# Optimization experiments

Hardware: AMD Instinct MI355X
Metric: run time of the kernel (lower is better)

Reference implementation:

```python
import jax, jax.numpy as jnp
import numpy as np

N = 5000  # num_nodes = feature dim = num classes
E = 160000


def _gcn_conv(x, src, dst, W, b, n):
    # PyG GCNConv: h = D^{-1/2} (A + I) D^{-1/2} (x W) + b
    h = x @ W  # [n, out]
    loops = jnp.arange(n, dtype=src.dtype)
    s = jnp.concatenate([src, loops])
    d = jnp.concatenate([dst, loops])
    deg = jax.ops.segment_sum(jnp.ones_like(s, dtype=h.dtype), d, num_segments=n)
    inv_sqrt = jnp.where(deg > 0, jax.lax.rsqrt(deg), 0.0)
    coef = inv_sqrt[s] * inv_sqrt[d]  # [E+n]
    msgs = h[s] * coef[:, None]       # gather-scale
    out = jax.ops.segment_sum(msgs, d, num_segments=n)  # scatter-add
    return out + b


def setup_inputs() -> dict:
    key = jax.random.key(0)
    k1, k2, k3, k4, k5 = jax.random.split(key, 5)
    x = jax.random.normal(k1, (N, N), dtype=jnp.float32)
    src = jax.random.randint(k2, (E,), 0, N, dtype=jnp.int32)
    dst = jax.random.randint(k3, (E,), 0, N, dtype=jnp.int32)
    W1 = jax.random.normal(k4, (N, 16), dtype=jnp.float32) * (1.0 / np.sqrt(N))
    b1 = jnp.zeros((16,), dtype=jnp.float32)
    W2 = jax.random.normal(k5, (16, N), dtype=jnp.float32) * (1.0 / np.sqrt(16))
    b2 = jnp.zeros((N,), dtype=jnp.float32)
    return {"x": x, "src": src, "dst": dst, "W1": W1, "b1": b1, "W2": W2, "b2": b2}


def reference(x, src, dst, W1, b1, W2, b2):
    h = _gcn_conv(x, src, dst, W1, b1, N)
    h = jax.nn.relu(h)
    h = _gcn_conv(h, src, dst, W2, b2, N)
    return jax.nn.log_softmax(h, axis=1)
```

## Files before the change

kernel.cpp:

```cpp
#include <hip/hip_runtime.h>
#include <math.h>

#define NN 5000
#define NE 160000
#define NF 16
#define CK 256


__global__ void k_deg(const int* __restrict__ dst, float* __restrict__ deg) {
  int t = blockIdx.x * 256 + threadIdx.x;
  if (t < NE) atomicAdd(&deg[dst[t]], 1.0f);
}

__global__ void k_inv(float* __restrict__ deg) {
  int v = blockIdx.x * 256 + threadIdx.x;
  if (v < NN) deg[v] = rsqrtf(deg[v] + 1.0f);
}

__global__ __launch_bounds__(256) void k_gemm1(const float* __restrict__ x,
                                               const float* __restrict__ w1,
                                               float* __restrict__ h1) {
  __shared__ float xs[16 * CK];
  __shared__ float ws[CK * NF];
  const int tid = threadIdx.x;
  const int lane = tid & 63;
  const int wv = tid >> 6;
  const int kk = lane >> 2;
  const int jq = lane & 3;
  const int rowbase = blockIdx.x * 16;
  const int kbeg = blockIdx.y * 1252;
  const int kend = (kbeg + 1252 < NN) ? kbeg + 1252 : NN;

  float acc[16];
#pragma unroll
  for (int i = 0; i < 16; ++i) acc[i] = 0.f;

  const int srow = tid >> 4;
  const int sf4 = tid & 15;
  const int grow = rowbase + srow;
  const float* __restrict__ xrow = x + (size_t)grow * NN;

  for (int kc = kbeg; kc < kend; kc += CK) {
    __syncthreads();
#pragma unroll
    for (int p = 0; p < 4; ++p) {
      const int s4 = sf4 + 16 * p;
      const int col = kc + s4 * 4;
      float4 v = make_float4(0.f, 0.f, 0.f, 0.f);
      if (grow < NN && col + 4 <= kend) v = *(const float4*)(xrow + col);
      *(float4*)(&xs[srow * CK + s4 * 4]) = v;
    }
    {
      const int k = kc + tid;
      if (k < kend) {
        const float4* __restrict__ wr = (const float4*)(w1 + (size_t)k * NF);
#pragma unroll
        for (int q = 0; q < 4; ++q) *(float4*)(&ws[tid * NF + q * 4]) = wr[q];
      } else {
#pragma unroll
        for (int q = 0; q < 4; ++q)
          *(float4*)(&ws[tid * NF + q * 4]) = make_float4(0.f, 0.f, 0.f, 0.f);
      }
    }
    __syncthreads();
    const float* __restrict__ xb = &xs[(wv * 4) * CK + kk];
    const float* __restrict__ wb = &ws[kk * NF + jq * 4];
#pragma unroll
    for (int c = 0; c < 16; ++c) {
      const float4 w4 = *(const float4*)(wb + c * (16 * NF));
      const float x0 = xb[0 * CK + c * 16];
      const float x1 = xb[1 * CK + c * 16];
      const float x2 = xb[2 * CK + c * 16];
      const float x3 = xb[3 * CK + c * 16];
      acc[0] = fmaf(x0, w4.x, acc[0]);  acc[1] = fmaf(x0, w4.y, acc[1]);
      acc[2] = fmaf(x0, w4.z, acc[2]);  acc[3] = fmaf(x0, w4.w, acc[3]);
      acc[4] = fmaf(x1, w4.x, acc[4]);  acc[5] = fmaf(x1, w4.y, acc[5]);
      acc[6] = fmaf(x1, w4.z, acc[6]);  acc[7] = fmaf(x1, w4.w, acc[7]);
      acc[8] = fmaf(x2, w4.x, acc[8]);  acc[9] = fmaf(x2, w4.y, acc[9]);
      acc[10] = fmaf(x2, w4.z, acc[10]); acc[11] = fmaf(x2, w4.w, acc[11]);
      acc[12] = fmaf(x3, w4.x, acc[12]); acc[13] = fmaf(x3, w4.y, acc[13]);
      acc[14] = fmaf(x3, w4.z, acc[14]); acc[15] = fmaf(x3, w4.w, acc[15]);
    }
  }

  int len = 16;
#pragma unroll
  for (int m = 32; m >= 4; m >>= 1) {
    len >>= 1;
    const bool hi = (lane & m) != 0;
#pragma unroll
    for (int i = 0; i < len; ++i) {
      float keep = hi ? acc[i + len] : acc[i];
      float give = hi ? acc[i] : acc[i + len];
      acc[i] = keep + __shfl_xor(give, m);
    }
  }
  const int r = kk >> 2, jj = kk & 3;
  const int row = rowbase + wv * 4 + r;
  if (row < NN) atomicAdd(&h1[row * NF + jq * 4 + jj], acc[0]);
}

__global__ void k_self(const float* __restrict__ h1, const float* __restrict__ inv,
                       float* __restrict__ g1) {
  int t = blockIdx.x * 256 + threadIdx.x;
  if (t >= NN * NF) return;
  float iv = inv[t >> 4];
  g1[t] = iv * iv * h1[t];
}

__global__ void k_edge(const int* __restrict__ src, const int* __restrict__ dst,
                       const float* __restrict__ inv, const float* __restrict__ hin,
                       float* __restrict__ gout) {
  int t = blockIdx.x * 256 + threadIdx.x;
  int e = t >> 4, j = t & 15;
  int s = src[e], d = dst[e];
  float c = inv[s] * inv[d];
  atomicAdd(&gout[d * NF + j], c * hin[s * NF + j]);
}

__global__ void k_relu2(const float* __restrict__ g1, const float* __restrict__ b1,
                        const float* __restrict__ inv, float* __restrict__ a1,
                        float* __restrict__ g2) {
  int t = blockIdx.x * 256 + threadIdx.x;
  if (t >= NN * NF) return;
  int v = t >> 4, j = t & 15;
  float a = fmaxf(g1[t] + b1[j], 0.f);
  a1[t] = a;
  float iv = inv[v];
  g2[t] = iv * iv * a;
}

__global__ __launch_bounds__(512) void k_final(const float* __restrict__ g2,
                                               const float* __restrict__ w2,
                                               const float* __restrict__ b2,
                                               float* __restrict__ out) {
  __shared__ float zs[4 * NN];
  __shared__ float gsh[64];
  __shared__ float red[8 * 4];
  __shared__ float rowmax[4];
  __shared__ float rowoff[4];
  const int tid = threadIdx.x;
  const int lane = tid & 63;
  const int wv = tid >> 6;
  const int row0 = blockIdx.x * 4;

  if (tid < 64) gsh[tid] = g2[row0 * NF + tid];
  __syncthreads();
  float g[4][NF];
#pragma unroll
  for (int r = 0; r < 4; ++r)
#pragma unroll
    for (int k = 0; k < NF; ++k) g[r][k] = gsh[r * NF + k];

  float mx[4] = {-1e30f, -1e30f, -1e30f, -1e30f};
  for (int jc = tid; jc < NN; jc += 512) {
    float w[NF];
#pragma unroll
    for (int k = 0; k < NF; ++k) w[k] = w2[k * NN + jc];
    const float bb = b2[jc];
#pragma unroll
    for (int r = 0; r < 4; ++r) {
      float z = bb;
#pragma unroll
      for (int k = 0; k < NF; ++k) z = fmaf(g[r][k], w[k], z);
      zs[r * NN + jc] = z;
      mx[r] = fmaxf(mx[r], z);
    }
  }
#pragma unroll
  for (int r = 0; r < 4; ++r) {
    float m = mx[r];
    for (int off = 32; off; off >>= 1) m = fmaxf(m, __shfl_xor(m, off));
    if (lane == 0) red[wv * 4 + r] = m;
  }
  __syncthreads();
  if (tid < 4) {
    float m = red[tid];
#pragma unroll
    for (int w = 1; w < 8; ++w) m = fmaxf(m, red[w * 4 + tid]);
    rowmax[tid] = m;
  }
  __syncthreads();
  const float rm0 = rowmax[0], rm1 = rowmax[1], rm2 = rowmax[2], rm3 = rowmax[3];

  float sm[4] = {0.f, 0.f, 0.f, 0.f};
  for (int jc = tid; jc < NN; jc += 512) {
    sm[0] += __expf(zs[0 * NN + jc] - rm0);
    sm[1] += __expf(zs[1 * NN + jc] - rm1);
    sm[2] += __expf(zs[2 * NN + jc] - rm2);
    sm[3] += __expf(zs[3 * NN + jc] - rm3);
  }
#pragma unroll
  for (int r = 0; r < 4; ++r) {
    float s = sm[r];
    for (int off = 32; off; off >>= 1) s += __shfl_xor(s, off);
    if (lane == 0) red[wv * 4 + r] = s;
  }
  __syncthreads();
  if (tid < 4) {
    float s = red[tid];
#pragma unroll
    for (int w = 1; w < 8; ++w) s += red[w * 4 + tid];
    rowoff[tid] = rowmax[tid] + logf(s);
  }
  __syncthreads();
  const float o0 = rowoff[0], o1 = rowoff[1], o2 = rowoff[2], o3 = rowoff[3];
  for (int jc = tid; jc < NN; jc += 512) {
    out[(size_t)(row0 + 0) * NN + jc] = zs[0 * NN + jc] - o0;
    out[(size_t)(row0 + 1) * NN + jc] = zs[1 * NN + jc] - o1;
    out[(size_t)(row0 + 2) * NN + jc] = zs[2 * NN + jc] - o2;
    out[(size_t)(row0 + 3) * NN + jc] = zs[3 * NN + jc] - o3;
  }
}

extern "C" void kernel_launch(void* const* d_in, const int* in_sizes, int n_in,
                              void* d_out, int out_size, void* d_ws, size_t ws_size,
                              hipStream_t stream) {
  const float* x  = (const float*)d_in[0];
  const int*   src = (const int*)d_in[1];
  const int*   dst = (const int*)d_in[2];
  const float* W1 = (const float*)d_in[3];
  const float* b1 = (const float*)d_in[4];
  const float* W2 = (const float*)d_in[5];
  const float* b2 = (const float*)d_in[6];
  float* out = (float*)d_out;

  char* ws = (char*)d_ws;
  float* deg = (float*)(ws);
  float* h1  = (float*)(ws + 20480);
  float* g1  = (float*)(ws + 340480);
  float* a1  = (float*)(ws + 660480);
  float* g2  = (float*)(ws + 980480);

  hipMemsetAsync(d_ws, 0, 340480, stream);
  k_deg<<<(NE + 255) / 256, 256, 0, stream>>>(dst, deg);
  k_inv<<<(NN + 255) / 256, 256, 0, stream>>>(deg);
  k_gemm1<<<dim3(313, 4), 256, 0, stream>>>(x, W1, h1);
  k_self<<<(NN * NF + 255) / 256, 256, 0, stream>>>(h1, deg, g1);
  k_edge<<<(NE * NF) / 256, 256, 0, stream>>>(src, dst, deg, h1, g1);
  k_relu2<<<(NN * NF + 255) / 256, 256, 0, stream>>>(g1, b1, deg, a1, g2);
  k_edge<<<(NE * NF) / 256, 256, 0, stream>>>(src, dst, deg, a1, g2);
  k_final<<<NN / 4, 512, 0, stream>>>(g2, W2, b2, out);
}
```

Before: 286.5 us.

## Stream x directly from global in GEMM1 and pad the W1 shared tile

After: 305.5 us. 1.07x slower.

```diff
diff --git a/kernel.cpp b/kernel.cpp
--- a/kernel.cpp
+++ b/kernel.cpp
@@ -5,6 +5,7 @@
 #define NE 160000
 #define NF 16
 #define CK 256
+#define WSTRIDE 20
 
 
 __global__ void k_deg(const int* __restrict__ dst, float* __restrict__ deg) {
@@ -20,84 +21,107 @@
 __global__ __launch_bounds__(256) void k_gemm1(const float* __restrict__ x,
                                                const float* __restrict__ w1,
                                                float* __restrict__ h1) {
-  __shared__ float xs[16 * CK];
-  __shared__ float ws[CK * NF];
+  __shared__ float ws2[CK * WSTRIDE];
   const int tid = threadIdx.x;
   const int lane = tid & 63;
   const int wv = tid >> 6;
-  const int kk = lane >> 2;
-  const int jq = lane & 3;
-  const int rowbase = blockIdx.x * 16;
-  const int kbeg = blockIdx.y * 1252;
-  const int kend = (kbeg + 1252 < NN) ? kbeg + 1252 : NN;
-
-  float acc[16];
-#pragma unroll
-  for (int i = 0; i < 16; ++i) acc[i] = 0.f;
-
-  const int srow = tid >> 4;
-  const int sf4 = tid & 15;
-  const int grow = rowbase + srow;
-  const float* __restrict__ xrow = x + (size_t)grow * NN;
+  const int row0 = blockIdx.x * 16 + wv * 4;
+  const int kbeg = blockIdx.y * 1280;
+  const int kend = (kbeg + 1280 < NN) ? kbeg + 1280 : NN;
+
+  float acc[4][NF];
+#pragma unroll
+  for (int r = 0; r < 4; ++r)
+#pragma unroll
+    for (int j = 0; j < NF; ++j) acc[r][j] = 0.f;
+
+  const float* __restrict__ xr0 = x + (size_t)((row0 + 0 < NN) ? row0 + 0 : NN - 1) * NN;
+  const float* __restrict__ xr1 = x + (size_t)((row0 + 1 < NN) ? row0 + 1 : NN - 1) * NN;
+  const float* __restrict__ xr2 = x + (size_t)((row0 + 2 < NN) ? row0 + 2 : NN - 1) * NN;
+  const float* __restrict__ xr3 = x + (size_t)((row0 + 3 < NN) ? row0 + 3 : NN - 1) * NN;
 
   for (int kc = kbeg; kc < kend; kc += CK) {
     __syncthreads();
-#pragma unroll
-    for (int p = 0; p < 4; ++p) {
-      const int s4 = sf4 + 16 * p;
-      const int col = kc + s4 * 4;
-      float4 v = make_float4(0.f, 0.f, 0.f, 0.f);
-      if (grow < NN && col + 4 <= kend) v = *(const float4*)(xrow + col);
-      *(float4*)(&xs[srow * CK + s4 * 4]) = v;
-    }
     {
       const int k = kc + tid;
+      float4 a = make_float4(0.f, 0.f, 0.f, 0.f), b = a, c = a, d = a;
       if (k < kend) {
         const float4* __restrict__ wr = (const float4*)(w1 + (size_t)k * NF);
-#pragma unroll
-        for (int q = 0; q < 4; ++q) *(float4*)(&ws[tid * NF + q * 4]) = wr[q];
-      } else {
-#pragma unroll
-        for (int q = 0; q < 4; ++q)
-          *(float4*)(&ws[tid * NF + q * 4]) = make_float4(0.f, 0.f, 0.f, 0.f);
+        a = wr[0]; b = wr[1]; c = wr[2]; d = wr[3];
       }
+      float* dp = &ws2[tid * WSTRIDE];
+      *(float4*)(dp + 0) = a;  *(float4*)(dp + 4) = b;
+      *(float4*)(dp + 8) = c;  *(float4*)(dp + 12) = d;
     }
     __syncthreads();
-    const float* __restrict__ xb = &xs[(wv * 4) * CK + kk];
-    const float* __restrict__ wb = &ws[kk * NF + jq * 4];
-#pragma unroll
-    for (int c = 0; c < 16; ++c) {
-      const float4 w4 = *(const float4*)(wb + c * (16 * NF));
-      const float x0 = xb[0 * CK + c * 16];
-      const float x1 = xb[1 * CK + c * 16];
-      const float x2 = xb[2 * CK + c * 16];
-      const float x3 = xb[3 * CK + c * 16];
-      acc[0] = fmaf(x0, w4.x, acc[0]);  acc[1] = fmaf(x0, w4.y, acc[1]);
-      acc[2] = fmaf(x0, w4.z, acc[2]);  acc[3] = fmaf(x0, w4.w, acc[3]);
-      acc[4] = fmaf(x1, w4.x, acc[4]);  acc[5] = fmaf(x1, w4.y, acc[5]);
-      acc[6] = fmaf(x1, w4.z, acc[6]);  acc[7] = fmaf(x1, w4.w, acc[7]);
-      acc[8] = fmaf(x2, w4.x, acc[8]);  acc[9] = fmaf(x2, w4.y, acc[9]);
-      acc[10] = fmaf(x2, w4.z, acc[10]); acc[11] = fmaf(x2, w4.w, acc[11]);
-      acc[12] = fmaf(x3, w4.x, acc[12]); acc[13] = fmaf(x3, w4.y, acc[13]);
-      acc[14] = fmaf(x3, w4.z, acc[14]); acc[15] = fmaf(x3, w4.w, acc[15]);
-    }
-  }
-
-  int len = 16;
-#pragma unroll
-  for (int m = 32; m >= 4; m >>= 1) {
-    len >>= 1;
-    const bool hi = (lane & m) != 0;
-#pragma unroll
-    for (int i = 0; i < len; ++i) {
-      float keep = hi ? acc[i + len] : acc[i];
-      float give = hi ? acc[i] : acc[i + len];
-      acc[i] = keep + __shfl_xor(give, m);
-    }
-  }
-  const int r = kk >> 2, jj = kk & 3;
-  const int row = rowbase + wv * 4 + r;
-  if (row < NN) atomicAdd(&h1[row * NF + jq * 4 + jj], acc[0]);
+#pragma unroll
+    for (int s = 0; s < 4; ++s) {
+      const int kl = s * 64 + lane;
+      int k = kc + kl;
+      if (k > NN - 1) k = NN - 1;
+      const float x0 = xr0[k];
+      const float x1 = xr1[k];
+      const float x2 = xr2[k];
+      const float x3 = xr3[k];
+      const float* __restrict__ wp = &ws2[kl * WSTRIDE];
+      const float4 w0 = *(const float4*)(wp + 0);
+      const float4 w1v = *(const float4*)(wp + 4);
+      const float4 w2v = *(const float4*)(wp + 8);
+      const float4 w3v = *(const float4*)(wp + 12);
+#pragma unroll
+      for (int r = 0; r < 4; ++r) {
+        const float xv = (r == 0) ? x0 : (r == 1) ? x1 : (r == 2) ? x2 : x3;
+        acc[r][0] = fmaf(xv, w0.x, acc[r][0]);
+        acc[r][1] = fmaf(xv, w0.y, acc[r][1]);
+        acc[r][2] = fmaf(xv, w0.z, acc[r][2]);
+        acc[r][3] = fmaf(xv, w0.w, acc[r][3]);
+        acc[r][4] = fmaf(xv, w1v.x, acc[r][4]);
+        acc[r][5] = fmaf(xv, w1v.y, acc[r][5]);
+        acc[r][6] = fmaf(xv, w1v.z, acc[r][6]);
+        acc[r][7] = fmaf(xv, w1v.w, acc[r][7]);
+        acc[r][8] = fmaf(xv, w2v.x, acc[r][8]);
+        acc[r][9] = fmaf(xv, w2v.y, acc[r][9]);
+        acc[r][10] = fmaf(xv, w2v.z, acc[r][10]);
+        acc[r][11] = fmaf(xv, w2v.w, acc[r][11]);
+        acc[r][12] = fmaf(xv, w3v.x, acc[r][12]);
+        acc[r][13] = fmaf(xv, w3v.y, acc[r][13]);
+        acc[r][14] = fmaf(xv, w3v.z, acc[r][14]);
+        acc[r][15] = fmaf(xv, w3v.w, acc[r][15]);
+      }
+    }
+  }
+
+  float tot[4];
+#pragma unroll
+  for (int r = 0; r < 4; ++r) {
+    float v[16];
+#pragma unroll
+    for (int j = 0; j < 16; ++j) v[j] = acc[r][j];
+    int len = 16;
+#pragma unroll
+    for (int m = 32; m >= 4; m >>= 1) {
+      len >>= 1;
+      const bool hi = (lane & m) != 0;
+#pragma unroll
+      for (int i = 0; i < len; ++i) {
+        float keep = hi ? v[i + len] : v[i];
+        float give = hi ? v[i] : v[i + len];
+        v[i] = keep + __shfl_xor(give, m);
+      }
+    }
+    float s = v[0];
+    s += __shfl_xor(s, 1);
+    s += __shfl_xor(s, 2);
+    tot[r] = s;
+  }
+  const int kk = (lane >> 2) & 15;
+  const int jq = lane & 3;
+  float val = tot[0];
+  if (jq == 1) val = tot[1];
+  if (jq == 2) val = tot[2];
+  if (jq == 3) val = tot[3];
+  const int row = row0 + jq;
+  if (row < NN) atomicAdd(&h1[row * NF + kk], val);
 }
 
 __global__ void k_self(const float* __restrict__ h1, const float* __restrict__ inv,
```
